# Performance work log

Measured on AMD Instinct MI355X. Metric: run time of the kernel, lower is better.

## Reference

```python
import jax, jax.numpy as jnp
from jax import lax
import numpy as np

DIM = 8          # per-head dim
BN_EPS = 1e-5
ATT_EPS = 1e-15


def setup_inputs() -> dict:
    key = jax.random.key(0)
    ks = jax.random.split(key, 6)
    B, C, H, W = 2, 512, 128, 128
    total_dim = 512                      # heads(64) * dim(8)
    c3 = 3 * total_dim                   # 1536
    x = jax.random.normal(ks[0], (B, C, H, W), dtype=jnp.float32)
    w_qkv = jax.random.normal(ks[1], (c3, C), dtype=jnp.float32) * 0.02
    w_dw = jax.random.normal(ks[2], (c3, 1, 5, 5), dtype=jnp.float32) * 0.05
    w_pw = jax.random.normal(ks[3], (c3, 8, 1, 1), dtype=jnp.float32) * 0.1
    w_proj = jax.random.normal(ks[4], (512, 2 * total_dim), dtype=jnp.float32) * 0.02
    bn_gamma = jnp.ones((512,), jnp.float32)
    bn_beta = jnp.zeros((512,), jnp.float32)
    bn_mean = jnp.zeros((512,), jnp.float32)
    bn_var = jnp.ones((512,), jnp.float32)
    return {"x": x, "w_qkv": w_qkv, "w_dw": w_dw, "w_pw": w_pw, "w_proj": w_proj,
            "bn_gamma": bn_gamma, "bn_beta": bn_beta, "bn_mean": bn_mean, "bn_var": bn_var}


def reference(x, w_qkv, w_dw, w_pw, w_proj, bn_gamma, bn_beta, bn_mean, bn_var):
    B, C, H, W = x.shape
    dn = ('NCHW', 'OIHW', 'NCHW')
    # qkv: 1x1 conv, no bias/norm/act
    qkv = jnp.einsum('bchw,oc->bohw', x, w_qkv)  # (B, 1536, H, W)
    # multi-scale aggregation: 5x5 depthwise + 1x1 grouped (groups = 3*heads = 192)
    y = lax.conv_general_dilated(qkv, w_dw, (1, 1), [(2, 2), (2, 2)],
                                 feature_group_count=w_dw.shape[0], dimension_numbers=dn)
    y = lax.conv_general_dilated(y, w_pw, (1, 1), [(0, 0), (0, 0)],
                                 feature_group_count=w_pw.shape[0] // w_pw.shape[1],
                                 dimension_numbers=dn)
    mqkv = jnp.concatenate([qkv, y], axis=1)  # (B, 3072, H, W)
    N = H * W
    mqkv = mqkv.reshape(B, -1, 3 * DIM, N)    # (B, 128 heads, 24, N)
    q = jax.nn.relu(mqkv[:, :, :DIM])          # (B, h, d, N)
    k = jax.nn.relu(mqkv[:, :, DIM:2 * DIM])   # (B, h, d, N)
    v = mqkv[:, :, 2 * DIM:]                   # (B, h, d, N)
    v = jnp.pad(v, ((0, 0), (0, 0), (0, 1), (0, 0)), constant_values=1.0)  # (B,h,d+1,N)
    vk = jnp.einsum('bhdn,bhen->bhde', v, k)   # v @ k^T : (B,h,d+1,d)
    out = jnp.einsum('bhde,bhen->bhdn', vk, q)  # (B,h,d+1,N)
    out = out[:, :, :-1] / (out[:, :, -1:] + ATT_EPS)  # (B,h,d,N)
    out = out.reshape(B, -1, H, W)             # (B, 1024, H, W)
    # proj: 1x1 conv + bn2d (inference-mode affine), no act
    out = jnp.einsum('bchw,oc->bohw', out, w_proj)
    inv = bn_gamma / jnp.sqrt(bn_var + BN_EPS)
    out = out * inv[None, :, None, None] + (bn_beta - bn_mean * inv)[None, :, None, None]
    return out
```

## Files before the change

kernel.cpp:

```cpp
#include <hip/hip_runtime.h>

typedef __bf16 bf16_t;
typedef __bf16 bf16x8 __attribute__((ext_vector_type(8)));
typedef __bf16 bf16x4 __attribute__((ext_vector_type(4)));
typedef __bf16 bf16x2 __attribute__((ext_vector_type(2)));
typedef float  f32x4  __attribute__((ext_vector_type(4)));

#define DEVINL __device__ __forceinline__

static constexpr size_t N_PIX = 16384;

static constexpr size_t OFF_Q   = 0;
static constexpr size_t SZ_Q    = (size_t)512 * N_PIX * 4;
static constexpr size_t OFF_QB  = OFF_Q + SZ_Q;
static constexpr size_t SZ_QB   = (size_t)512 * N_PIX * 2;
static constexpr size_t OFF_KV  = OFF_QB + SZ_QB;
static constexpr size_t SZ_KV   = (size_t)1024 * N_PIX * 2;
static constexpr size_t OFF_Y   = OFF_KV + SZ_KV;
static constexpr size_t SZ_Y    = (size_t)1536 * N_PIX * 2;
static constexpr size_t OFF_ATT = OFF_Y + SZ_Y;
static constexpr size_t SZ_ATT  = (size_t)N_PIX * 1024 * 2;
static constexpr size_t OFF_XTH = OFF_ATT;
static constexpr size_t OFF_XTL = OFF_ATT + (size_t)N_PIX * 512 * 2;
static constexpr size_t OFF_WQA = OFF_ATT + SZ_ATT;
static constexpr size_t SZ_WQA  = (size_t)512 * 1536 * 2;
static constexpr size_t OFF_WKV = OFF_WQA + SZ_WQA;
static constexpr size_t SZ_WKV  = (size_t)1024 * 512 * 2;
static constexpr size_t OFF_WP  = OFF_WKV + SZ_WKV;
static constexpr size_t SZ_WP   = (size_t)512 * 1024 * 2;
static constexpr size_t OFF_VK  = OFF_WP + SZ_WP;
static constexpr size_t SZ_VK   = (size_t)128 * 72 * 4;
static constexpr size_t OFF_VKP = OFF_VK + SZ_VK;
static constexpr size_t SZ_VKP  = (size_t)128 * 8 * 72 * 4;
static constexpr size_t OFF_BNA = OFF_VKP + SZ_VKP;
static constexpr size_t OFF_ZP  = OFF_BNA + 2048;
static constexpr size_t WS_NEEDED = OFF_ZP + 64;

DEVINL void gload16(const bf16_t* g, bf16_t* l) {
  __builtin_amdgcn_global_load_lds((const __attribute__((address_space(1))) void*)g,
                                   (__attribute__((address_space(3))) void*)l, 16, 0, 0);
}

__global__ __launch_bounds__(256)
void xpose_kernel(const float* __restrict__ x, bf16_t* __restrict__ xTh, bf16_t* __restrict__ xTl) {
  __shared__ float t[32][33];
  const int n0 = blockIdx.x * 32, c0 = blockIdx.y * 32;
  const int tx = threadIdx.x & 31, ty = threadIdx.x >> 5;
#pragma unroll
  for (int r = 0; r < 4; ++r)
    t[ty + r * 8][tx] = x[(size_t)(c0 + ty + r * 8) * N_PIX + n0 + tx];
  __syncthreads();
#pragma unroll
  for (int r = 0; r < 4; ++r) {
    const float v = t[tx][ty + r * 8];
    const bf16_t hi = (bf16_t)v;
    const bf16_t lo = (bf16_t)(v - (float)hi);
    const size_t o = (size_t)(n0 + ty + r * 8) * 512 + c0 + tx;
    xTh[o] = hi; xTl[o] = lo;
  }
}

static constexpr int PREP_W1 = 512 * 1536;
static constexpr int PREP_W2 = 1024 * 512;
static constexpr int PREP_W3 = 512 * 1024;
static constexpr int PREP_TOT = PREP_W1 + PREP_W2 + PREP_W3 + 512 + 16;
__global__ __launch_bounds__(256)
void prep_kernel(const float* __restrict__ wq, const float* __restrict__ wp,
                 const float* __restrict__ gam, const float* __restrict__ bet,
                 const float* __restrict__ mu, const float* __restrict__ va,
                 bf16_t* __restrict__ wqA, bf16_t* __restrict__ wkv, bf16_t* __restrict__ wpb,
                 float* __restrict__ bna, float* __restrict__ zp) {
  const int i = blockIdx.x * 256 + threadIdx.x;
  if (i < PREP_W1) {
    const int r = i / 1536, c = i - r * 1536;
    const int o = (r >> 3) * 24 + (r & 7);
    bf16_t out;
    if (c < 512) {
      out = (bf16_t)wq[o * 512 + c];
    } else if (c < 1024) {
      const float v = wq[o * 512 + c - 512];
      const bf16_t hi = (bf16_t)v;
      out = (bf16_t)(v - (float)hi);
    } else {
      out = (bf16_t)wq[o * 512 + c - 1024];
    }
    wqA[i] = out;
  } else if (i < PREP_W1 + PREP_W2) {
    const int j = i - PREP_W1;
    const int r = j >> 9, c = j & 511;
    const int h = (r & 511) >> 3;
    const int jj = (r < 512 ? 8 : 16) + (r & 7);
    wkv[j] = (bf16_t)wq[(h * 24 + jj) * 512 + c];
  } else if (i < PREP_W1 + PREP_W2 + PREP_W3) {
    const int j = i - PREP_W1 - PREP_W2;
    const int m = j >> 10;
    const float inv = gam[m] / sqrtf(va[m] + 1e-5f);
    wpb[j] = (bf16_t)(wp[j] * inv);
  } else if (i < PREP_W1 + PREP_W2 + PREP_W3 + 512) {
    const int k = i - PREP_W1 - PREP_W2 - PREP_W3;
    const float inv = gam[k] / sqrtf(va[k] + 1e-5f);
    bna[k] = bet[k] - mu[k] * inv;
  } else if (i < PREP_TOT) {
    zp[i - (PREP_W1 + PREP_W2 + PREP_W3 + 512)] = 0.f;
  }
}

__global__ __launch_bounds__(256, 4)
void gemm_qkv_kernel(const bf16_t* __restrict__ wqA, const bf16_t* __restrict__ wkv,
                     const bf16_t* __restrict__ xTh, const bf16_t* __restrict__ xTl,
                     float* __restrict__ Qf, bf16_t* __restrict__ Qb, bf16_t* __restrict__ KV) {
  __shared__ __align__(16) bf16_t As[128 * 64];
  __shared__ __align__(16) bf16_t Bs[128 * 64];
  const int tid = threadIdx.x, wid = tid >> 6, lane = tid & 63;
  const int fr = lane & 15, fg = lane >> 4;
  const int wm = (wid >> 1) * 64, wn = (wid & 1) * 64;
  const int by = blockIdx.y;
  const bool isQ = by < 4;
  const int m0 = (isQ ? by : by - 4) * 128;
  const int n0 = blockIdx.x * 128;
  const int KA = isQ ? 1536 : 512;
  const bf16_t* Aptr = isQ ? wqA + (size_t)m0 * 1536 : wkv + (size_t)m0 * 512;
  const int srow = tid >> 3;
  const int soff = (((tid & 7) ^ (srow & 7)) * 8);

  f32x4 acc[4][4] = {};

  for (int kk = 0; kk < KA; kk += 64) {
    const bf16_t* Bpl;
    int bcol;
    if (isQ) {
      Bpl  = (kk < 1024) ? xTh : xTl;
      bcol = (kk < 1024) ? (kk & 511) : (kk - 1024);
    } else {
      Bpl = xTh; bcol = kk;
    }
    __syncthreads();
#pragma unroll
    for (int r = 0; r < 4; ++r) {
      gload16(Aptr + (size_t)(srow + 32 * r) * KA + kk + soff, As + (wid * 8 + 32 * r) * 64);
      gload16(Bpl + (size_t)(n0 + srow + 32 * r) * 512 + bcol + soff, Bs + (wid * 8 + 32 * r) * 64);
    }
    __syncthreads();
#pragma unroll
    for (int ks = 0; ks < 2; ++ks) {
      bf16x8 af[4], bfr[4];
#pragma unroll
      for (int i = 0; i < 4; ++i)
        af[i]  = *(const bf16x8*)&As[(wm + i * 16 + fr) * 64 + (((ks * 4 + fg) ^ (fr & 7)) * 8)];
#pragma unroll
      for (int j = 0; j < 4; ++j)
        bfr[j] = *(const bf16x8*)&Bs[(wn + j * 16 + fr) * 64 + (((ks * 4 + fg) ^ (fr & 7)) * 8)];
#pragma unroll
      for (int i = 0; i < 4; ++i)
#pragma unroll
        for (int j = 0; j < 4; ++j)
          acc[i][j] = __builtin_amdgcn_mfma_f32_16x16x32_bf16(af[i], bfr[j], acc[i][j], 0, 0, 0);
    }
  }

#pragma unroll
  for (int i = 0; i < 4; ++i)
#pragma unroll
    for (int r = 0; r < 4; ++r) {
      const int m = m0 + wm + i * 16 + fg * 4 + r;
#pragma unroll
      for (int j = 0; j < 4; ++j) {
        const int n = n0 + wn + j * 16 + fr;
        const float v = acc[i][j][r];
        if (isQ) {
          Qf[(size_t)m * N_PIX + n] = v;
          Qb[(size_t)m * N_PIX + n] = (bf16_t)v;
        } else {
          KV[(size_t)m * N_PIX + n] = (bf16_t)v;
        }
      }
    }
}

__global__ __launch_bounds__(256, 4)
void gemm_proj_kernel(const bf16_t* __restrict__ A, const bf16_t* __restrict__ B,
                      float* __restrict__ Cout, const float* __restrict__ bna) {
  __shared__ __align__(16) bf16_t As[128 * 64];
  __shared__ __align__(16) bf16_t Bs[128 * 64];
  const int tid = threadIdx.x, wid = tid >> 6, lane = tid & 63;
  const int fr = lane & 15, fg = lane >> 4;
  const int wm = (wid >> 1) * 64, wn = (wid & 1) * 64;
  const int m0 = blockIdx.y * 128, n0 = blockIdx.x * 128;
  const int srow = tid >> 3;
  const int soff = (((tid & 7) ^ (srow & 7)) * 8);
  const bf16_t* Ab = A + (size_t)m0 * 1024;
  const bf16_t* Bb = B + (size_t)n0 * 1024;

  f32x4 acc[4][4] = {};

  for (int kk = 0; kk < 1024; kk += 64) {
    __syncthreads();
#pragma unroll
    for (int r = 0; r < 4; ++r) {
      gload16(Ab + (size_t)(srow + 32 * r) * 1024 + kk + soff, As + (wid * 8 + 32 * r) * 64);
      gload16(Bb + (size_t)(srow + 32 * r) * 1024 + kk + soff, Bs + (wid * 8 + 32 * r) * 64);
    }
    __syncthreads();
#pragma unroll
    for (int ks = 0; ks < 2; ++ks) {
      bf16x8 af[4], bfr[4];
#pragma unroll
      for (int i = 0; i < 4; ++i)
        af[i]  = *(const bf16x8*)&As[(wm + i * 16 + fr) * 64 + (((ks * 4 + fg) ^ (fr & 7)) * 8)];
#pragma unroll
      for (int j = 0; j < 4; ++j)
        bfr[j] = *(const bf16x8*)&Bs[(wn + j * 16 + fr) * 64 + (((ks * 4 + fg) ^ (fr & 7)) * 8)];
#pragma unroll
      for (int i = 0; i < 4; ++i)
#pragma unroll
        for (int j = 0; j < 4; ++j)
          acc[i][j] = __builtin_amdgcn_mfma_f32_16x16x32_bf16(af[i], bfr[j], acc[i][j], 0, 0, 0);
    }
  }

#pragma unroll
  for (int i = 0; i < 4; ++i)
#pragma unroll
    for (int r = 0; r < 4; ++r) {
      const int m = m0 + wm + i * 16 + fg * 4 + r;
      const float sh = bna[m];
#pragma unroll
      for (int j = 0; j < 4; ++j)
        Cout[(size_t)m * N_PIX + n0 + wn + j * 16 + fr] = acc[i][j][r] + sh;
    }
}

__global__ __launch_bounds__(256)
void dwpw_kernel(const bf16_t* __restrict__ Qb, const bf16_t* __restrict__ KV,
                 const float* __restrict__ wdw, const float* __restrict__ wpw,
                 const bf16_t* __restrict__ zp, bf16_t* __restrict__ y) {
  const int g = blockIdx.y, t = blockIdx.x;
  const int typ = g % 3, head = g / 3;
  const int ty0 = (t >> 1) * 16, tx0 = (t & 1) * 64;
  const int tid = threadIdx.x, wid = tid >> 6, lane = tid & 63;
  __shared__ __align__(16) bf16_t sin_[8][20][80];
  __shared__ float swd[8][25];
  __shared__ float swp[8][8];
  if (tid < 200) swd[tid / 25][tid % 25] = wdw[(g * 8 + tid / 25) * 25 + tid % 25];
  if (tid < 64)  swp[tid >> 3][tid & 7] = wpw[(g * 8 + (tid >> 3)) * 8 + (tid & 7)];
  const bf16_t* plane = (typ == 0) ? (Qb + (size_t)head * 8 * N_PIX)
                                   : (KV + (size_t)((typ == 2 ? 512 : 0) + head * 8) * N_PIX);
  bf16_t* sflat = &sin_[0][0][0];
  for (int base = wid * 64; base < 1600; base += 256) {
    const int id  = base + lane;
    const int ch  = id / 200;
    const int rem = id - ch * 200;
    const int row = rem / 10;
    const int c6  = rem - row * 10;
    const int gy  = ty0 + row - 2;
    const int gx  = tx0 + c6 * 8 - 8;
    const bool ok = ((unsigned)gy < 128u) && ((unsigned)gx < 128u);
    const bf16_t* src = ok ? (plane + (size_t)ch * N_PIX + gy * 128 + gx) : zp;
    gload16(src, sflat + (size_t)base * 8);
  }
  __syncthreads();

  const int px4 = (tid & 15) * 4, py = tid >> 4;
  float dwres[8][4];
#pragma unroll
  for (int ch = 0; ch < 8; ++ch) {
    float o0 = 0.f, o1 = 0.f, o2 = 0.f, o3 = 0.f;
#pragma unroll
    for (int di = 0; di < 5; ++di) {
      bf16x4 a0 = *(const bf16x4*)&sin_[ch][py + di][px4 + 4];
      bf16x4 a1 = *(const bf16x4*)&sin_[ch][py + di][px4 + 8];
      bf16x4 a2 = *(const bf16x4*)&sin_[ch][py + di][px4 + 12];
      float vv[12] = {(float)a0[0], (float)a0[1], (float)a0[2], (float)a0[3],
                      (float)a1[0], (float)a1[1], (float)a1[2], (float)a1[3],
                      (float)a2[0], (float)a2[1], (float)a2[2], (float)a2[3]};
#pragma unroll
      for (int dj = 0; dj < 5; ++dj) {
        const float w = swd[ch][di * 5 + dj];
        o0 += vv[dj + 2] * w; o1 += vv[dj + 3] * w;
        o2 += vv[dj + 4] * w; o3 += vv[dj + 5] * w;
      }
    }
    dwres[ch][0] = o0; dwres[ch][1] = o1; dwres[ch][2] = o2; dwres[ch][3] = o3;
  }
#pragma unroll
  for (int oc = 0; oc < 8; ++oc) {
    float o[4] = {0.f, 0.f, 0.f, 0.f};
#pragma unroll
    for (int ic = 0; ic < 8; ++ic) {
      const float w = swp[oc][ic];
#pragma unroll
      for (int u = 0; u < 4; ++u) o[u] += dwres[ic][u] * w;
    }
    bf16x4 ov;
#pragma unroll
    for (int u = 0; u < 4; ++u) ov[u] = (bf16_t)o[u];
    *(bf16x4*)&y[(size_t)(8 * g + oc) * N_PIX + (ty0 + py) * 128 + tx0 + px4] = ov;
  }
}

__global__ __launch_bounds__(256)
void vk_partial_kernel(const bf16_t* __restrict__ KV, const bf16_t* __restrict__ yb,
                       float* __restrict__ part) {
  const int h = blockIdx.y, s = blockIdx.x;
  const bf16_t *kb, *vb;
  if (h < 64) {
    kb = KV + (size_t)(h * 8) * N_PIX;
    vb = KV + (size_t)(512 + h * 8) * N_PIX;
  } else {
    kb = yb + (size_t)(24 * (h - 64) + 8) * N_PIX;
    vb = yb + (size_t)(24 * (h - 64) + 16) * N_PIX;
  }
  float a[8][8] = {};
  float ak[8] = {};
  const int p0 = s * 2048 + (int)threadIdx.x * 2;
  for (int it = 0; it < 4; ++it) {
    const int p = p0 + it * 512;
    float k0[8], k1[8], v0[8], v1[8];
#pragma unroll
    for (int e = 0; e < 8; ++e) {
      bf16x2 kk = *(const bf16x2*)&kb[(size_t)e * N_PIX + p];
      k0[e] = fmaxf(0.f, (float)kk[0]); k1[e] = fmaxf(0.f, (float)kk[1]);
    }
#pragma unroll
    for (int d = 0; d < 8; ++d) {
      bf16x2 vv = *(const bf16x2*)&vb[(size_t)d * N_PIX + p];
      v0[d] = (float)vv[0]; v1[d] = (float)vv[1];
    }
#pragma unroll
    for (int d = 0; d < 8; ++d)
#pragma unroll
      for (int e = 0; e < 8; ++e) {
        a[d][e] += v0[d] * k0[e];
        a[d][e] += v1[d] * k1[e];
      }
#pragma unroll
    for (int e = 0; e < 8; ++e) ak[e] += k0[e] + k1[e];
  }
  __shared__ float red[4][72];
  const int lane = threadIdx.x & 63, wid = threadIdx.x >> 6;
#pragma unroll
  for (int i = 0; i < 72; ++i) {
    float v = (i < 64) ? a[i >> 3][i & 7] : ak[i - 64];
    v += __shfl_xor(v, 32); v += __shfl_xor(v, 16); v += __shfl_xor(v, 8);
    v += __shfl_xor(v, 4);  v += __shfl_xor(v, 2);  v += __shfl_xor(v, 1);
    if (lane == 0) red[wid][i] = v;
  }
  __syncthreads();
  if (threadIdx.x < 72) {
    const float sum_ = red[0][threadIdx.x] + red[1][threadIdx.x] + red[2][threadIdx.x] + red[3][threadIdx.x];
    part[((size_t)h * 8 + s) * 72 + threadIdx.x] = sum_;
  }
}

__global__ __launch_bounds__(128)
void vk_reduce_kernel(const float* __restrict__ part, float* __restrict__ vk) {
  const int h = blockIdx.x;
  const int i = threadIdx.x;
  if (i < 72) {
    float s = 0.f;
#pragma unroll
    for (int t = 0; t < 8; ++t) s += part[((size_t)h * 8 + t) * 72 + i];
    vk[(size_t)h * 72 + i] = s;
  }
}

__global__ __launch_bounds__(256)
void attn_kernel(const float* __restrict__ Qf, const bf16_t* __restrict__ yb,
                 const float* __restrict__ vk, bf16_t* __restrict__ attT) {
  const int n0 = blockIdx.x * 32;
  const int tid = threadIdx.x;
  const int px = tid & 31, hl = tid >> 5;
  __shared__ __align__(16) bf16_t att_s[32 * 512];
  __shared__ float vk_s[576];
  for (int grp = 0; grp < 2; ++grp) {
    for (int hg = 0; hg < 8; ++hg) {
      __syncthreads();
      for (int i = tid; i < 576; i += 256)
        vk_s[i] = vk[((size_t)grp * 64 + hg * 8) * 72 + i];
      __syncthreads();
      const int hh = hg * 8 + hl;
      float q[8];
      if (grp == 0) {
        const float* plane = Qf + (size_t)(hh * 8) * N_PIX + n0 + px;
#pragma unroll
        for (int e = 0; e < 8; ++e) q[e] = fmaxf(0.f, plane[(size_t)e * N_PIX]);
      } else {
        const bf16_t* plane = yb + (size_t)(24 * hh) * N_PIX + n0 + px;
#pragma unroll
        for (int e = 0; e < 8; ++e) q[e] = fmaxf(0.f, (float)plane[(size_t)e * N_PIX]);
      }
      float den = 1e-15f;
#pragma unroll
      for (int e = 0; e < 8; ++e) den += vk_s[hl * 72 + 64 + e] * q[e];
      const float rden = 1.0f / den;
      bf16x8 r8;
#pragma unroll
      for (int d = 0; d < 8; ++d) {
        float num = 0.f;
#pragma unroll
        for (int e = 0; e < 8; ++e) num += vk_s[hl * 72 + d * 8 + e] * q[e];
        r8[d] = (bf16_t)(num * rden);
      }
      const int chunk = hg * 8 + hl;
      *(bf16x8*)&att_s[px * 512 + ((chunk ^ (px & 7)) << 3)] = r8;
    }
    __syncthreads();
    bf16_t* dst = attT + (size_t)n0 * 1024 + grp * 512;
    for (int i = tid; i < 2048; i += 256) {
      const int r = i >> 6, cc = i & 63;
      bf16x8 v = *(const bf16x8*)&att_s[r * 512 + (((cc ^ (r & 7))) << 3)];
      *(bf16x8*)&dst[(size_t)r * 1024 + cc * 8] = v;
    }
  }
}

extern "C" void kernel_launch(void* const* d_in, const int* in_sizes, int n_in,
                              void* d_out, int out_size, void* d_ws, size_t ws_size,
                              hipStream_t stream) {
  if (ws_size < WS_NEEDED) return;
  const float* x      = (const float*)d_in[0];
  const float* w_qkv  = (const float*)d_in[1];
  const float* w_dw   = (const float*)d_in[2];
  const float* w_pw   = (const float*)d_in[3];
  const float* w_proj = (const float*)d_in[4];
  const float* gam    = (const float*)d_in[5];
  const float* bet    = (const float*)d_in[6];
  const float* mu     = (const float*)d_in[7];
  const float* va     = (const float*)d_in[8];

  char* w = (char*)d_ws;
  float*  Qf   = (float*)(w + OFF_Q);
  bf16_t* Qb   = (bf16_t*)(w + OFF_QB);
  bf16_t* KV   = (bf16_t*)(w + OFF_KV);
  bf16_t* yb   = (bf16_t*)(w + OFF_Y);
  bf16_t* xTh  = (bf16_t*)(w + OFF_XTH);
  bf16_t* xTl  = (bf16_t*)(w + OFF_XTL);
  bf16_t* attT = (bf16_t*)(w + OFF_ATT);
  bf16_t* wqA  = (bf16_t*)(w + OFF_WQA);
  bf16_t* wkv  = (bf16_t*)(w + OFF_WKV);
  bf16_t* wpb  = (bf16_t*)(w + OFF_WP);
  float*  vk   = (float*)(w + OFF_VK);
  float*  part = (float*)(w + OFF_VKP);
  float*  bna  = (float*)(w + OFF_BNA);
  float*  zp   = (float*)(w + OFF_ZP);

  dim3 blk(256);
  prep_kernel<<<dim3((PREP_TOT + 255) / 256), blk, 0, stream>>>(
      w_qkv, w_proj, gam, bet, mu, va, wqA, wkv, wpb, bna, zp);

  for (int b = 0; b < 2; ++b) {
    const float* xb = x + (size_t)b * 512 * N_PIX;
    float* outb = (float*)d_out + (size_t)b * 512 * N_PIX;
    xpose_kernel<<<dim3(512, 16), blk, 0, stream>>>(xb, xTh, xTl);
    gemm_qkv_kernel<<<dim3(128, 12), blk, 0, stream>>>(wqA, wkv, xTh, xTl, Qf, Qb, KV);
    dwpw_kernel<<<dim3(16, 192), blk, 0, stream>>>(Qb, KV, w_dw, w_pw, (const bf16_t*)zp, yb);
    vk_partial_kernel<<<dim3(8, 128), blk, 0, stream>>>(KV, yb, part);
    vk_reduce_kernel<<<dim3(128), dim3(128), 0, stream>>>(part, vk);
    attn_kernel<<<dim3(512), blk, 0, stream>>>(Qf, yb, vk, attT);
    gemm_proj_kernel<<<dim3(128, 4), blk, 0, stream>>>(wpb, attT, outb, bna);
  }
}
```

Baseline: 380.4 us.

## Vectorize xpose stores, double-buffer dwpw tiles, widen vk_partial loads

```diff
diff --git a/kernel.cpp b/kernel.cpp
--- a/kernel.cpp
+++ b/kernel.cpp
@@ -50,14 +50,21 @@
   for (int r = 0; r < 4; ++r)
     t[ty + r * 8][tx] = x[(size_t)(c0 + ty + r * 8) * N_PIX + n0 + tx];
   __syncthreads();
-#pragma unroll
-  for (int r = 0; r < 4; ++r) {
-    const float v = t[tx][ty + r * 8];
-    const bf16_t hi = (bf16_t)v;
-    const bf16_t lo = (bf16_t)(v - (float)hi);
-    const size_t o = (size_t)(n0 + ty + r * 8) * 512 + c0 + tx;
-    xTh[o] = hi; xTl[o] = lo;
-  }
+  const int nl = threadIdx.x >> 3, sub = threadIdx.x & 7;
+  const int c8 = (sub & 3) * 8, plane = sub >> 2;
+  bf16x8 o;
+#pragma unroll
+  for (int k = 0; k < 8; ++k) {
+    const float v = t[c8 + k][nl];
+    if (plane == 0) {
+      o[k] = (bf16_t)v;
+    } else {
+      const bf16_t hi = (bf16_t)v;
+      o[k] = (bf16_t)(v - (float)hi);
+    }
+  }
+  bf16_t* dst = plane ? xTl : xTh;
+  *(bf16x8*)&dst[(size_t)(n0 + nl) * 512 + c0 + c8] = o;
 }
 
 static constexpr int PREP_W1 = 512 * 1536;
@@ -234,67 +241,80 @@
 void dwpw_kernel(const bf16_t* __restrict__ Qb, const bf16_t* __restrict__ KV,
                  const float* __restrict__ wdw, const float* __restrict__ wpw,
                  const bf16_t* __restrict__ zp, bf16_t* __restrict__ y) {
-  const int g = blockIdx.y, t = blockIdx.x;
+  const int g = blockIdx.y;
   const int typ = g % 3, head = g / 3;
-  const int ty0 = (t >> 1) * 16, tx0 = (t & 1) * 64;
+  const int r0 = blockIdx.x * 32;
   const int tid = threadIdx.x, wid = tid >> 6, lane = tid & 63;
-  __shared__ __align__(16) bf16_t sin_[8][20][80];
+  __shared__ __align__(16) bf16_t sbuf[2][8][20][80];
   __shared__ float swd[8][25];
   __shared__ float swp[8][8];
   if (tid < 200) swd[tid / 25][tid % 25] = wdw[(g * 8 + tid / 25) * 25 + tid % 25];
   if (tid < 64)  swp[tid >> 3][tid & 7] = wpw[(g * 8 + (tid >> 3)) * 8 + (tid & 7)];
   const bf16_t* plane = (typ == 0) ? (Qb + (size_t)head * 8 * N_PIX)
                                    : (KV + (size_t)((typ == 2 ? 512 : 0) + head * 8) * N_PIX);
-  bf16_t* sflat = &sin_[0][0][0];
-  for (int base = wid * 64; base < 1600; base += 256) {
-    const int id  = base + lane;
-    const int ch  = id / 200;
-    const int rem = id - ch * 200;
-    const int row = rem / 10;
-    const int c6  = rem - row * 10;
-    const int gy  = ty0 + row - 2;
-    const int gx  = tx0 + c6 * 8 - 8;
-    const bool ok = ((unsigned)gy < 128u) && ((unsigned)gx < 128u);
-    const bf16_t* src = ok ? (plane + (size_t)ch * N_PIX + gy * 128 + gx) : zp;
-    gload16(src, sflat + (size_t)base * 8);
-  }
+
+  auto stage = [&](int t, int buf) {
+    const int ty0 = r0 + (t >> 1) * 16, tx0 = (t & 1) * 64;
+    bf16_t* sf = &sbuf[buf][0][0][0];
+    for (int base = wid * 64; base < 1600; base += 256) {
+      const int id  = base + lane;
+      const int ch  = id / 200;
+      const int rem = id - ch * 200;
+      const int row = rem / 10;
+      const int c6  = rem - row * 10;
+      const int gy  = ty0 + row - 2;
+      const int gx  = tx0 + c6 * 8 - 8;
+      const bool ok = ((unsigned)gy < 128u) && ((unsigned)gx < 128u);
+      const bf16_t* src = ok ? (plane + (size_t)ch * N_PIX + gy * 128 + gx) : zp;
+      gload16(src, sf + (size_t)base * 8);
+    }
+  };
+
+  stage(0, 0);
   __syncthreads();
 
   const int px4 = (tid & 15) * 4, py = tid >> 4;
-  float dwres[8][4];
-#pragma unroll
-  for (int ch = 0; ch < 8; ++ch) {
-    float o0 = 0.f, o1 = 0.f, o2 = 0.f, o3 = 0.f;
-#pragma unroll
-    for (int di = 0; di < 5; ++di) {
-      bf16x4 a0 = *(const bf16x4*)&sin_[ch][py + di][px4 + 4];
-      bf16x4 a1 = *(const bf16x4*)&sin_[ch][py + di][px4 + 8];
-      bf16x4 a2 = *(const bf16x4*)&sin_[ch][py + di][px4 + 12];
-      float vv[12] = {(float)a0[0], (float)a0[1], (float)a0[2], (float)a0[3],
-                      (float)a1[0], (float)a1[1], (float)a1[2], (float)a1[3],
-                      (float)a2[0], (float)a2[1], (float)a2[2], (float)a2[3]};
-#pragma unroll
-      for (int dj = 0; dj < 5; ++dj) {
-        const float w = swd[ch][di * 5 + dj];
-        o0 += vv[dj + 2] * w; o1 += vv[dj + 3] * w;
-        o2 += vv[dj + 4] * w; o3 += vv[dj + 5] * w;
+#pragma unroll
+  for (int t = 0; t < 4; ++t) {
+    if (t < 3) stage(t + 1, (t + 1) & 1);
+    const int ty0 = r0 + (t >> 1) * 16, tx0 = (t & 1) * 64;
+    const int cb = t & 1;
+    float dwres[8][4];
+#pragma unroll
+    for (int ch = 0; ch < 8; ++ch) {
+      float o0 = 0.f, o1 = 0.f, o2 = 0.f, o3 = 0.f;
+#pragma unroll
+      for (int di = 0; di < 5; ++di) {
+        bf16x4 a0 = *(const bf16x4*)&sbuf[cb][ch][py + di][px4 + 4];
+        bf16x4 a1 = *(const bf16x4*)&sbuf[cb][ch][py + di][px4 + 8];
+        bf16x4 a2 = *(const bf16x4*)&sbuf[cb][ch][py + di][px4 + 12];
+        float vv[12] = {(float)a0[0], (float)a0[1], (float)a0[2], (float)a0[3],
+                        (float)a1[0], (float)a1[1], (float)a1[2], (float)a1[3],
+                        (float)a2[0], (float)a2[1], (float)a2[2], (float)a2[3]};
+#pragma unroll
+        for (int dj = 0; dj < 5; ++dj) {
+          const float w = swd[ch][di * 5 + dj];
+          o0 += vv[dj + 2] * w; o1 += vv[dj + 3] * w;
+          o2 += vv[dj + 4] * w; o3 += vv[dj + 5] * w;
+        }
       }
-    }
-    dwres[ch][0] = o0; dwres[ch][1] = o1; dwres[ch][2] = o2; dwres[ch][3] = o3;
-  }
-#pragma unroll
-  for (int oc = 0; oc < 8; ++oc) {
-    float o[4] = {0.f, 0.f, 0.f, 0.f};
-#pragma unroll
-    for (int ic = 0; ic < 8; ++ic) {
-      const float w = swp[oc][ic];
-#pragma unroll
-      for (int u = 0; u < 4; ++u) o[u] += dwres[ic][u] * w;
-    }
-    bf16x4 ov;
-#pragma unroll
-    for (int u = 0; u < 4; ++u) ov[u] = (bf16_t)o[u];
-    *(bf16x4*)&y[(size_t)(8 * g + oc) * N_PIX + (ty0 + py) * 128 + tx0 + px4] = ov;
+      dwres[ch][0] = o0; dwres[ch][1] = o1; dwres[ch][2] = o2; dwres[ch][3] = o3;
+    }
+#pragma unroll
+    for (int oc = 0; oc < 8; ++oc) {
+      float o[4] = {0.f, 0.f, 0.f, 0.f};
+#pragma unroll
+      for (int ic = 0; ic < 8; ++ic) {
+        const float w = swp[oc][ic];
+#pragma unroll
+        for (int u = 0; u < 4; ++u) o[u] += dwres[ic][u] * w;
+      }
+      bf16x4 ov;
+#pragma unroll
+      for (int u = 0; u < 4; ++u) ov[u] = (bf16_t)o[u];
+      *(bf16x4*)&y[(size_t)(8 * g + oc) * N_PIX + (ty0 + py) * 128 + tx0 + px4] = ov;
+    }
+    if (t < 3) __syncthreads();
   }
 }
 
@@ -312,29 +332,32 @@
   }
   float a[8][8] = {};
   float ak[8] = {};
-  const int p0 = s * 2048 + (int)threadIdx.x * 2;
-  for (int it = 0; it < 4; ++it) {
-    const int p = p0 + it * 512;
-    float k0[8], k1[8], v0[8], v1[8];
+  const int p0 = s * 2048 + (int)threadIdx.x * 4;
+  for (int it = 0; it < 2; ++it) {
+    const int p = p0 + it * 1024;
+    float kq[8][4], vq[8][4];
 #pragma unroll
     for (int e = 0; e < 8; ++e) {
-      bf16x2 kk = *(const bf16x2*)&kb[(size_t)e * N_PIX + p];
-      k0[e] = fmaxf(0.f, (float)kk[0]); k1[e] = fmaxf(0.f, (float)kk[1]);
+      bf16x4 kk = *(const bf16x4*)&kb[(size_t)e * N_PIX + p];
+#pragma unroll
+      for (int u = 0; u < 4; ++u) kq[e][u] = fmaxf(0.f, (float)kk[u]);
     }
 #pragma unroll
     for (int d = 0; d < 8; ++d) {
-      bf16x2 vv = *(const bf16x2*)&vb[(size_t)d * N_PIX + p];
-      v0[d] = (float)vv[0]; v1[d] = (float)vv[1];
+      bf16x4 vv = *(const bf16x4*)&vb[(size_t)d * N_PIX + p];
+#pragma unroll
+      for (int u = 0; u < 4; ++u) vq[d][u] = (float)vv[u];
     }
 #pragma unroll
     for (int d = 0; d < 8; ++d)
 #pragma unroll
-      for (int e = 0; e < 8; ++e) {
-        a[d][e] += v0[d] * k0[e];
-        a[d][e] += v1[d] * k1[e];
-      }
-#pragma unroll
-    for (int e = 0; e < 8; ++e) ak[e] += k0[e] + k1[e];
+      for (int e = 0; e < 8; ++e)
+#pragma unroll
+        for (int u = 0; u < 4; ++u) a[d][e] += vq[d][u] * kq[e][u];
+#pragma unroll
+    for (int e = 0; e < 8; ++e)
+#pragma unroll
+      for (int u = 0; u < 4; ++u) ak[e] += kq[e][u];
   }
   __shared__ float red[4][72];
   const int lane = threadIdx.x & 63, wid = threadIdx.x >> 6;
@@ -453,7 +476,7 @@
     float* outb = (float*)d_out + (size_t)b * 512 * N_PIX;
     xpose_kernel<<<dim3(512, 16), blk, 0, stream>>>(xb, xTh, xTl);
     gemm_qkv_kernel<<<dim3(128, 12), blk, 0, stream>>>(wqA, wkv, xTh, xTl, Qf, Qb, KV);
-    dwpw_kernel<<<dim3(16, 192), blk, 0, stream>>>(Qb, KV, w_dw, w_pw, (const bf16_t*)zp, yb);
+    dwpw_kernel<<<dim3(4, 192), blk, 0, stream>>>(Qb, KV, w_dw, w_pw, (const bf16_t*)zp, yb);
     vk_partial_kernel<<<dim3(8, 128), blk, 0, stream>>>(KV, yb, part);
     vk_reduce_kernel<<<dim3(128), dim3(128), 0, stream>>>(part, vk);
     attn_kernel<<<dim3(512), blk, 0, stream>>>(Qf, yb, vk, attT);
```

New measurement: 426.2 us. 12.0% more time.
